# Kernel tuning notes

Hardware: AMD Instinct MI355X
Metric: run time of the kernel (lower is better)

Reference implementation:

```python
import jax, jax.numpy as jnp
import numpy as np

B, NQ, C, H0, NKPT, NH, NS = 8, 100, 768, 64, 17, 8, 3
HID = 4 * C
SIGMAS = (0.05, 0.15, 0.3)


def _ln(x, g, b):
    m = jnp.mean(x, -1, keepdims=True)
    v = jnp.mean((x - m) ** 2, -1, keepdims=True)
    return (x - m) / jnp.sqrt(v + 1e-5) * g + b


def _bias(kpts, H, W, sigma):
    # kpts: [B,N,2] normalized xy; returns additive bias [B,1,1,H*W]
    k = jnp.clip(kpts, 0.0, 1.0)
    ys, xs = jnp.meshgrid(jnp.arange(H, dtype=k.dtype), jnp.arange(W, dtype=k.dtype), indexing='ij')
    grid = jnp.stack([xs / (W - 1), ys / (H - 1)], -1).reshape(1, 1, H * W, 2)
    d = jnp.sum((k[:, :, None, :] - grid) ** 2, -1)  # [B,N,HW]
    m = jnp.min(d, axis=1)                           # [B,HW] min over keypoints
    return jnp.maximum(-(m / (2.0 * sigma * sigma)), -10000.0)[:, None, None, :]


def _attn(q, kv, Wq, bq, Wk, bk, Wv, bv, Wo, bo, bias, h):
    Bq, Nq, Cd = q.shape
    d = Cd // h
    scale = d ** -0.5
    qh = (q @ Wq + bq).reshape(Bq, Nq, h, d).transpose(0, 2, 1, 3)
    kh = (kv @ Wk + bk).reshape(Bq, -1, h, d).transpose(0, 2, 1, 3)
    vh = (kv @ Wv + bv).reshape(Bq, -1, h, d).transpose(0, 2, 1, 3)
    s = jnp.einsum('bhqd,bhkd->bhqk', qh, kh) * scale + bias
    a = jax.nn.softmax(s, axis=-1)
    o = jnp.einsum('bhqk,bhkd->bhqd', a, vh).transpose(0, 2, 1, 3).reshape(Bq, Nq, Cd)
    return o @ Wo + bo


def setup_inputs() -> dict:
    key = jax.random.key(0)
    def n(i, shape, sc=0.02):
        return jax.random.normal(jax.random.fold_in(key, i), shape, dtype=jnp.float32) * sc
    return dict(
        query_token=n(0, (B, NQ, C), 1.0),
        image_features=n(1, (B, C, H0, H0), 1.0),
        pose_kpts=jax.random.uniform(jax.random.fold_in(key, 2), (B, NKPT, 2), dtype=jnp.float32),
        norm_feat_g=jnp.ones((C,), jnp.float32), norm_feat_b=jnp.zeros((C,), jnp.float32),
        ds_w=n(3, (NS - 1, C, C, 2, 2)), ds_b=jnp.zeros((NS - 1, C), jnp.float32),
        q_w=n(4, (NS, C, C)), q_b=jnp.zeros((NS, C), jnp.float32),
        k_w=n(5, (NS, C, C)), k_b=jnp.zeros((NS, C), jnp.float32),
        v_w=n(6, (NS, C, C)), v_b=jnp.zeros((NS, C), jnp.float32),
        o_w=n(7, (NS, C, C)), o_b=jnp.zeros((NS, C), jnp.float32),
        scale_weights=jnp.ones((NS,), jnp.float32),
        norm_attn_g=jnp.ones((C,), jnp.float32), norm_attn_b=jnp.zeros((C,), jnp.float32),
        ffn_w1=n(8, (C, HID)), ffn_b1=jnp.zeros((HID,), jnp.float32),
        ffn_w2=n(9, (HID, C)), ffn_b2=jnp.zeros((C,), jnp.float32),
        norm_ffn_g=jnp.ones((C,), jnp.float32), norm_ffn_b=jnp.zeros((C,), jnp.float32),
    )


def reference(query_token, image_features, pose_kpts, norm_feat_g, norm_feat_b, ds_w, ds_b,
              q_w, q_b, k_w, k_b, v_w, v_b, o_w, o_b, scale_weights,
              norm_attn_g, norm_attn_b, ffn_w1, ffn_b1, ffn_w2, ffn_b2,
              norm_ffn_g, norm_ffn_b):
    w = jax.nn.softmax(scale_weights)
    curr = image_features
    fused = 0.0
    for i in range(NS):
        if i > 0:
            curr = jax.lax.conv_general_dilated(
                curr, ds_w[i - 1], (2, 2), 'VALID',
                dimension_numbers=('NCHW', 'OIHW', 'NCHW')) + ds_b[i - 1][None, :, None, None]
        Bc, Cc, Hc, Wc = curr.shape
        feat = _ln(curr.reshape(Bc, Cc, Hc * Wc).transpose(0, 2, 1), norm_feat_g, norm_feat_b)
        bias = _bias(pose_kpts, Hc, Wc, SIGMAS[min(i, len(SIGMAS) - 1)])
        fused = fused + w[i] * _attn(query_token, feat, q_w[i], q_b[i], k_w[i], k_b[i],
                                     v_w[i], v_b[i], o_w[i], o_b[i], bias, NH)
    x = _ln(query_token + fused, norm_attn_g, norm_attn_b)
    x = x + (jax.nn.relu(x @ ffn_w1 + ffn_b1) @ ffn_w2 + ffn_b2)
    return _ln(x, norm_ffn_g, norm_ffn_b)
```

## Files before the change

### kernel.cpp

```cpp
#include <hip/hip_runtime.h>
#include <stdint.h>


typedef unsigned short u16;
typedef __attribute__((ext_vector_type(4))) float f32x4;
typedef __attribute__((ext_vector_type(8))) short s16x8;
typedef __attribute__((ext_vector_type(4))) short s16x4;

#define DEVI static __device__ __forceinline__

DEVI float bf2f(u16 u){ union { unsigned int ui; float f; } v; v.ui = ((unsigned int)u)<<16; return v.f; }
DEVI u16 f2bf(float f){ union { float f; unsigned int ui; } v; v.f = f;
  unsigned int r = v.ui + 0x7FFFu + ((v.ui>>16)&1u); return (u16)(r>>16); }
DEVI f32x4 mfma_bf16(s16x8 a, s16x8 b, f32x4 c){
  return __builtin_amdgcn_mfma_f32_16x16x32_bf16(a,b,c,0,0,0);
}
DEVI void gload_lds16(const void* g, void* l){
  __builtin_amdgcn_global_load_lds((const __attribute__((address_space(1))) void*)g,
                                   (__attribute__((address_space(3))) void*)l, 16, 0, 0);
}


__global__ __launch_bounds__(64) void smax3_k(const float* __restrict__ sw, float* __restrict__ w3){
  if (threadIdx.x==0){
    float a=sw[0],b=sw[1],c=sw[2];
    float mx=fmaxf(a,fmaxf(b,c));
    float ea=__expf(a-mx), eb=__expf(b-mx), ec=__expf(c-mx);
    float inv=1.f/(ea+eb+ec);
    w3[0]=ea*inv; w3[1]=eb*inv; w3[2]=ec*inv;
  }
}

__global__ __launch_bounds__(256) void cvt_k(const float* __restrict__ in, u16* __restrict__ out, int n4){
  int i = blockIdx.x*256 + threadIdx.x;
  if (i>=n4) return;
  f32x4 v = *(const f32x4*)(in + (long)i*4);
  s16x4 o;
  o[0]=(short)f2bf(v[0]); o[1]=(short)f2bf(v[1]); o[2]=(short)f2bf(v[2]); o[3]=(short)f2bf(v[3]);
  *(s16x4*)(out + (long)i*4) = o;
}

__global__ __launch_bounds__(256) void tr_k(const float* __restrict__ in, u16* __restrict__ out, int R, int C){
  __shared__ float tile[32][33];
  long z = blockIdx.z;
  in  += z*(long)R*C;
  out += z*(long)R*C;
  int tx = threadIdx.x & 31, ty = threadIdx.x>>5;
  int r0 = blockIdx.y*32, c0 = blockIdx.x*32;
#pragma unroll
  for (int j=0;j<4;++j) tile[ty+j*8][tx] = in[(long)(r0+ty+j*8)*C + c0+tx];
  __syncthreads();
#pragma unroll
  for (int j=0;j<4;++j) out[(long)(c0+ty+j*8)*R + r0+tx] = f2bf(tile[tx][ty+j*8]);
}

__global__ __launch_bounds__(256) void convw_k(const float* __restrict__ dsw, u16* __restrict__ out){
  int i = blockIdx.x*256 + threadIdx.x;
  f32x4 v = *(const f32x4*)(dsw + (long)i*4);
  int s = i/(768*768); int rem = i - s*768*768;
  int o = rem/768; int ii = rem - o*768;
#pragma unroll
  for (int dyx=0;dyx<4;++dyx)
    out[(((long)s*4+dyx)*768 + o)*768 + ii] = f2bf(v[dyx]);
}

__global__ __launch_bounds__(256) void ln_bf16_k(const u16* __restrict__ in, u16* __restrict__ out,
    const float* __restrict__ g, const float* __restrict__ bt, int nrows){
  int w = threadIdx.x>>6, lane = threadIdx.x&63;
  long row = (long)blockIdx.x*4 + w;
  if (row >= nrows) return;
  const u16* rp = in + row*768;
  s16x8 v8 = *(const s16x8*)(rp + lane*8);
  s16x4 v4 = *(const s16x4*)(rp + 512 + lane*4);
  float x[12];
#pragma unroll
  for (int i=0;i<8;++i) x[i]   = bf2f((u16)v8[i]);
#pragma unroll
  for (int i=0;i<4;++i) x[8+i] = bf2f((u16)v4[i]);
  float s=0.f,s2=0.f;
#pragma unroll
  for (int i=0;i<12;++i){ s += x[i]; s2 += x[i]*x[i]; }
  for (int m=1;m<64;m<<=1){ s += __shfl_xor(s,m); s2 += __shfl_xor(s2,m); }
  float mean = s*(1.f/768.f);
  float var  = s2*(1.f/768.f) - mean*mean;
  float rstd = rsqrtf(fmaxf(var,0.f)+1e-5f);
  u16* op = out + row*768;
  s16x8 o8; s16x4 o4;
#pragma unroll
  for (int i=0;i<8;++i){ int c = lane*8+i;     o8[i] = (short)f2bf((x[i]-mean)*rstd*g[c]+bt[c]); }
#pragma unroll
  for (int i=0;i<4;++i){ int c = 512+lane*4+i; o4[i] = (short)f2bf((x[8+i]-mean)*rstd*g[c]+bt[c]); }
  *(s16x8*)(op + lane*8) = o8;
  *(s16x4*)(op + 512 + lane*4) = o4;
}

__global__ __launch_bounds__(256) void bias_k(const float* __restrict__ kpts, float* __restrict__ out,
    int HW, int log2W, float invWm1, float invHm1, float inv2s2){
  __shared__ float2 kp[17];
  int b = blockIdx.y;
  if (threadIdx.x < 17) kp[threadIdx.x] = ((const float2*)kpts)[b*17 + threadIdx.x];
  __syncthreads();
  int p = blockIdx.x*256 + threadIdx.x;
  int W = 1<<log2W;
  int y = p>>log2W, x = p&(W-1);
  float gx = x*invWm1, gy = y*invHm1;
  float m = 1e30f;
#pragma unroll 1
  for (int k=0;k<17;++k){
    float kx = fminf(fmaxf(kp[k].x,0.f),1.f) - gx;
    float ky = fminf(fmaxf(kp[k].y,0.f),1.f) - gy;
    m = fminf(m, kx*kx+ky*ky);
  }
  out[(long)b*HW + p] = fmaxf(-m*inv2s2, -10000.f);
}

template<int OUTM, bool RELU, bool QPAD, bool CONV>
__global__ __launch_bounds__(256,4) void gemm_k(
    const u16* __restrict__ A, const u16* __restrict__ Bt,
    const float* __restrict__ bias, void* __restrict__ Cout,
    int M, int N, int K,
    const float* __restrict__ alpha_ptr, int accum_init,
    int Win, int HWin, int log2Wout, int log2HWout, int ldct)
{
  __shared__ u16 As[2][128*32];
  __shared__ u16 Bs[2][128*32];
  const int t = threadIdx.x, lane = t&63, w = t>>6;
  const int wr = w>>1, wc = w&1;
  const int m0 = blockIdx.x*128, n0 = blockIdx.y*128;
  f32x4 acc[4][4];
  const f32x4 fz = {0.f,0.f,0.f,0.f};
#pragma unroll
  for (int i=0;i<4;++i)
#pragma unroll
    for (int j=0;j<4;++j) acc[i][j] = fz;

  const int nk = K>>5;
  const int nt = (CONV ? 4*nk : nk);

  auto stage = [&](int dyx, int k0, int b){
    const u16* Bp = CONV ? (Bt + (long)dyx*N*K) : Bt;
    const int dy = dyx>>1, dx = dyx&1;
#pragma unroll
    for (int p=0;p<2;++p){
      int f = p*256+t, r = f>>2, cv = f&3;
      int cvs = cv ^ ((r>>1)&3);
      int gm = m0 + r;
      long arow;
      if (CONV){
        int bb = gm >> log2HWout;
        int pp = gm & ((1<<log2HWout)-1);
        int yy = pp >> log2Wout, xx = pp & ((1<<log2Wout)-1);
        arow = (long)bb*HWin + (2*yy+dy)*Win + (2*xx+dx);
      } else arow = gm;
      gload_lds16(A + arow*(long)K + k0 + cvs*8, &As[b][(long)f*8]);
    }
#pragma unroll
    for (int p=0;p<2;++p){
      int f = p*256+t, r = f>>2, cv = f&3;
      int cvs = cv ^ ((r>>1)&3);
      gload_lds16(Bp + (long)(n0+r)*K + k0 + cvs*8, &Bs[b][(long)f*8]);
    }
  };

  stage(0, 0, 0);
  __syncthreads();

  int cur = 0, dyx = 0, kk = 0;
  for (int s = 0; s < nt; ++s){
    int nkk = kk + 1, ndx = dyx;
    if (nkk == nk){ nkk = 0; ndx = dyx + 1; }
    if (s + 1 < nt) stage(ndx, nkk<<5, cur^1);

    const int g16 = lane>>4, l16 = lane&15;
    s16x8 af[4], bf[4];
#pragma unroll
    for (int i=0;i<4;++i){
      int row = wr*64 + i*16 + l16;
      af[i] = *(const s16x8*)&As[cur][row*32 + ((g16 ^ ((row>>1)&3))*8)];
    }
#pragma unroll
    for (int j=0;j<4;++j){
      int row = wc*64 + j*16 + l16;
      bf[j] = *(const s16x8*)&Bs[cur][row*32 + ((g16 ^ ((row>>1)&3))*8)];
    }
#pragma unroll
    for (int i=0;i<4;++i)
#pragma unroll
      for (int j=0;j<4;++j)
        acc[i][j] = mfma_bf16(af[i], bf[j], acc[i][j]);

    __syncthreads();
    cur ^= 1; kk = nkk; dyx = ndx;
  }

  const int col16 = lane&15, g = lane>>4;
  float alpha = (OUTM==2) ? *alpha_ptr : 1.f;
#pragma unroll
  for (int i=0;i<4;++i){
    int rowbase = m0 + wr*64 + i*16 + g*4;
#pragma unroll
    for (int j=0;j<4;++j){
      int colg = n0 + wc*64 + j*16 + col16;
      float bv = bias ? bias[colg] : 0.f;
      f32x4 c = acc[i][j];
      if (OUTM==3){
        if (rowbase < M){
          int bb  = rowbase >> log2HWout;
          int pix = rowbase & ((1<<log2HWout)-1);
          s16x4 pk;
          pk[0]=(short)f2bf(c[0]+bv); pk[1]=(short)f2bf(c[1]+bv);
          pk[2]=(short)f2bf(c[2]+bv); pk[3]=(short)f2bf(c[3]+bv);
          *(s16x4*)((u16*)Cout + ((long)bb*768 + colg)*ldct + pix) = pk;
        }
      } else {
#pragma unroll
        for (int r=0;r<4;++r){
          int row = rowbase + r;
          if (row < M){
            float v = c[r] + bv;
            if (RELU) v = fmaxf(v, 0.f);
            if (OUTM==0){
              long orow = row;
              if (QPAD){ int bb = row/100; orow = bb*128 + (row - bb*100); }
              ((u16*)Cout)[orow*(long)N + colg] = f2bf(v);
            } else if (OUTM==1){
              ((float*)Cout)[(long)row*N + colg] = v;
            } else {
              float* p = (float*)Cout + (long)row*N + colg;
              *p = (accum_init ? 0.f : *p) + alpha*v;
            }
          }
        }
      }
    }
  }
}

__global__ __launch_bounds__(256,2) void attn_fwd_k(
    const u16* __restrict__ Qp, const u16* __restrict__ Kb,
    const u16* __restrict__ Vt, const float* __restrict__ biasb,
    float* __restrict__ Opart, float* __restrict__ mpart, float* __restrict__ lpart,
    int HW, int ntiles)
{
  __shared__ u16 Ps[4*32*64];
  const int t = threadIdx.x, lane = t&63, w = t>>6;
  const int col = lane&15, g = lane>>4;
  const int bh = blockIdx.x, b = bh>>3, h = bh&7, ch = blockIdx.y;
  const int kvbase = ch*ntiles*64;
  const int qrow = w*32;
  const u16* Qbase = Qp + (long)b*128*768 + h*96;
  const u16* Kbase = Kb + (long)b*HW*768 + h*96;
  const u16* Vbase = Vt + ((long)b*768 + h*96)*HW;
  const float* bb  = biasb + (long)b*HW;
  const float scale = 0.10206207261596575f;

  s16x8 qf[2][3];
#pragma unroll
  for (int qi=0;qi<2;++qi)
#pragma unroll
    for (int kf=0;kf<3;++kf)
      qf[qi][kf] = *(const s16x8*)(Qbase + (long)(qrow+qi*16+col)*768 + kf*32 + g*8);

  const f32x4 fz = {0.f,0.f,0.f,0.f};
  f32x4 of[2][6];
#pragma unroll
  for (int qi=0;qi<2;++qi)
#pragma unroll
    for (int nf=0;nf<6;++nf) of[qi][nf] = fz;
  float mrow[2][4], lrow[2][4];
#pragma unroll
  for (int qi=0;qi<2;++qi)
#pragma unroll
    for (int r=0;r<4;++r){ mrow[qi][r] = -1e30f; lrow[qi][r] = 0.f; }

  for (int ti=0; ti<ntiles; ++ti){
    const int kv0 = kvbase + ti*64;
    s16x8 kfr[4][3];
#pragma unroll
    for (int cf=0;cf<4;++cf)
#pragma unroll
      for (int kf=0;kf<3;++kf)
        kfr[cf][kf] = *(const s16x8*)(Kbase + (long)(kv0+cf*16+col)*768 + kf*32 + g*8);
    f32x4 sc[2][4];
#pragma unroll
    for (int qi=0;qi<2;++qi)
#pragma unroll
      for (int cf=0;cf<4;++cf) sc[qi][cf] = fz;
#pragma unroll
    for (int kf=0;kf<3;++kf)
#pragma unroll
      for (int qi=0;qi<2;++qi)
#pragma unroll
        for (int cf=0;cf<4;++cf)
          sc[qi][cf] = mfma_bf16(qf[qi][kf], kfr[cf][kf], sc[qi][cf]);
    float bv[4];
#pragma unroll
    for (int cf=0;cf<4;++cf) bv[cf] = bb[kv0+cf*16+col];

#pragma unroll
    for (int qi=0;qi<2;++qi){
      f32x4 sp[4];
#pragma unroll
      for (int cf=0;cf<4;++cf)
#pragma unroll
        for (int r=0;r<4;++r) sp[cf][r] = sc[qi][cf][r]*scale + bv[cf];
      f32x4 mx = sp[0];
#pragma unroll
      for (int cf=1;cf<4;++cf)
#pragma unroll
        for (int r=0;r<4;++r) mx[r] = fmaxf(mx[r], sp[cf][r]);
      for (int mm=1;mm<16;mm<<=1){
#pragma unroll
        for (int r=0;r<4;++r) mx[r] = fmaxf(mx[r], __shfl_xor(mx[r], mm));
      }
      float sf[4], mn[4];
#pragma unroll
      for (int r=0;r<4;++r){
        mn[r] = fmaxf(mrow[qi][r], mx[r]);
        sf[r] = __expf(mrow[qi][r]-mn[r]);
        mrow[qi][r] = mn[r];
      }
      f32x4 psum = fz;
#pragma unroll
      for (int cf=0;cf<4;++cf)
#pragma unroll
        for (int r=0;r<4;++r){ float p = __expf(sp[cf][r]-mn[r]); sp[cf][r]=p; psum[r]+=p; }
      for (int mm=1;mm<16;mm<<=1){
#pragma unroll
        for (int r=0;r<4;++r) psum[r] += __shfl_xor(psum[r], mm);
      }
#pragma unroll
      for (int r=0;r<4;++r) lrow[qi][r] = lrow[qi][r]*sf[r] + psum[r];
#pragma unroll
      for (int nf=0;nf<6;++nf)
#pragma unroll
        for (int r=0;r<4;++r) of[qi][nf][r] *= sf[r];
#pragma unroll
      for (int cf=0;cf<4;++cf)
#pragma unroll
        for (int r=0;r<4;++r){
          int lr = qi*16 + g*4 + r;
          int cc = cf*16 + col;
          int byteoff = (qrow + lr)*128 + ((cc*2) ^ ((lr&7)<<4));
          *(u16*)((char*)Ps + byteoff) = f2bf(sp[cf][r]);
        }
    }
#pragma unroll
    for (int k2=0;k2<2;++k2){
      s16x8 pa[2];
#pragma unroll
      for (int qi=0;qi<2;++qi){
        int lr = qi*16 + col;
        int byteoff = (qrow+lr)*128 + ((k2*64 + g*16) ^ ((lr&7)<<4));
        pa[qi] = *(const s16x8*)((const char*)Ps + byteoff);
      }
#pragma unroll
      for (int nf=0;nf<6;++nf){
        s16x8 vbf = *(const s16x8*)(Vbase + (long)(nf*16+col)*HW + kv0 + k2*32 + g*8);
#pragma unroll
        for (int qi=0;qi<2;++qi)
          of[qi][nf] = mfma_bf16(pa[qi], vbf, of[qi][nf]);
      }
    }
  }
  long obase = ((long)ch*64 + bh)*128;
#pragma unroll
  for (int qi=0;qi<2;++qi)
#pragma unroll
    for (int nf=0;nf<6;++nf)
#pragma unroll
      for (int r=0;r<4;++r)
        Opart[(obase + qrow + qi*16 + g*4 + r)*96L + nf*16 + col] = of[qi][nf][r];
  if (col==0){
#pragma unroll
    for (int qi=0;qi<2;++qi)
#pragma unroll
      for (int r=0;r<4;++r){
        int row = qrow + qi*16 + g*4 + r;
        mpart[obase+row] = mrow[qi][r];
        lpart[obase+row] = lrow[qi][r];
      }
  }
}

__global__ __launch_bounds__(128) void attn_comb_k(const float* __restrict__ Opart,
    const float* __restrict__ mpart, const float* __restrict__ lpart,
    u16* __restrict__ out, int nch){
  int bh = blockIdx.x, q = blockIdx.y, d = threadIdx.x;
  int b = bh>>3, h = bh&7;
  float M = -1e30f;
  for (int c=0;c<nch;++c) M = fmaxf(M, mpart[((long)c*64+bh)*128+q]);
  float L = 0.f, o = 0.f;
  for (int c=0;c<nch;++c){
    long base = ((long)c*64+bh)*128+q;
    float e = __expf(mpart[base]-M);
    L += lpart[base]*e;
    if (d<96) o += Opart[base*96+d]*e;
  }
  if (d<96) out[((long)(b*100+q))*768 + h*96 + d] = f2bf(o/L);
}

__global__ __launch_bounds__(256) void postattn_k(const float* __restrict__ q,
    const float* __restrict__ fus, const float* __restrict__ g, const float* __restrict__ bt,
    float* __restrict__ x1f, u16* __restrict__ x1b){
  int w = threadIdx.x>>6, lane = threadIdx.x&63;
  long row = (long)blockIdx.x*4 + w;
  const f32x4* qp = (const f32x4*)(q   + row*768);
  const f32x4* fp = (const f32x4*)(fus + row*768);
  f32x4 xv[3];
  float s=0.f,s2=0.f;
#pragma unroll
  for (int p=0;p<3;++p){
    f32x4 a = qp[p*64+lane], c = fp[p*64+lane];
    xv[p] = a + c;
#pragma unroll
    for (int r=0;r<4;++r){ s += xv[p][r]; s2 += xv[p][r]*xv[p][r]; }
  }
  for (int m=1;m<64;m<<=1){ s += __shfl_xor(s,m); s2 += __shfl_xor(s2,m); }
  float mean = s*(1.f/768.f);
  float var  = s2*(1.f/768.f) - mean*mean;
  float rstd = rsqrtf(fmaxf(var,0.f)+1e-5f);
#pragma unroll
  for (int p=0;p<3;++p){
    int c0 = (p*64+lane)*4;
    f32x4 o; s16x4 ob;
#pragma unroll
    for (int r=0;r<4;++r){ o[r] = (xv[p][r]-mean)*rstd*g[c0+r]+bt[c0+r]; ob[r]=(short)f2bf(o[r]); }
    *(f32x4*)(x1f + row*768 + c0) = o;
    *(s16x4*)(x1b + row*768 + c0) = ob;
  }
}

__global__ __launch_bounds__(256) void final_k(const float* __restrict__ x1f,
    const float* __restrict__ yb, const float* __restrict__ g, const float* __restrict__ bt,
    float* __restrict__ out){
  int w = threadIdx.x>>6, lane = threadIdx.x&63;
  long row = (long)blockIdx.x*4 + w;
  const f32x4* xp = (const f32x4*)(x1f + row*768);
  const f32x4* yp = (const f32x4*)(yb  + row*768);
  f32x4 xv[3];
  float s=0.f,s2=0.f;
#pragma unroll
  for (int p=0;p<3;++p){
    f32x4 a = xp[p*64+lane], c = yp[p*64+lane];
    xv[p] = a + c;
#pragma unroll
    for (int r=0;r<4;++r){ s += xv[p][r]; s2 += xv[p][r]*xv[p][r]; }
  }
  for (int m=1;m<64;m<<=1){ s += __shfl_xor(s,m); s2 += __shfl_xor(s2,m); }
  float mean = s*(1.f/768.f);
  float var  = s2*(1.f/768.f) - mean*mean;
  float rstd = rsqrtf(fmaxf(var,0.f)+1e-5f);
#pragma unroll
  for (int p=0;p<3;++p){
    int c0 = (p*64+lane)*4;
    f32x4 o;
#pragma unroll
    for (int r=0;r<4;++r) o[r] = (xv[p][r]-mean)*rstd*g[c0+r]+bt[c0+r];
    *(f32x4*)(out + row*768 + c0) = o;
  }
}

extern "C" void kernel_launch(void* const* d_in, const int* in_sizes, int n_in,
                              void* d_out, int out_size, void* d_ws, size_t ws_size,
                              hipStream_t stream)
{
  (void)in_sizes; (void)n_in; (void)out_size; (void)ws_size;
  const float* query = (const float*)d_in[0];
  const float* imgf  = (const float*)d_in[1];
  const float* kpts  = (const float*)d_in[2];
  const float* nfg   = (const float*)d_in[3];
  const float* nfb   = (const float*)d_in[4];
  const float* dsw   = (const float*)d_in[5];
  const float* dsb   = (const float*)d_in[6];
  const float* qw    = (const float*)d_in[7];
  const float* qbv   = (const float*)d_in[8];
  const float* kw    = (const float*)d_in[9];
  const float* kbv   = (const float*)d_in[10];
  const float* vw    = (const float*)d_in[11];
  const float* vbv   = (const float*)d_in[12];
  const float* ow    = (const float*)d_in[13];
  const float* obv   = (const float*)d_in[14];
  const float* sw    = (const float*)d_in[15];
  const float* nag   = (const float*)d_in[16];
  const float* nab   = (const float*)d_in[17];
  const float* fw1   = (const float*)d_in[18];
  const float* fb1   = (const float*)d_in[19];
  const float* fw2   = (const float*)d_in[20];
  const float* fb2   = (const float*)d_in[21];
  const float* ngg   = (const float*)d_in[22];
  const float* ngb   = (const float*)d_in[23];
  float* out = (float*)d_out;

  char* ws = (char*)d_ws;
  size_t off = 0;
  auto carve = [&](size_t bytes)->char*{
    off = (off + 255) & ~(size_t)255;
    char* p = ws + off; off += bytes; return p;
  };
  float* w3     = (float*)carve(16);
  u16* wq_t     = (u16*)carve(3UL*768*768*2);
  u16* wk_t     = (u16*)carve(3UL*768*768*2);
  u16* wv_t     = (u16*)carve(3UL*768*768*2);
  u16* wo_t     = (u16*)carve(3UL*768*768*2);
  u16* wf1_t    = (u16*)carve(3072UL*768*2);
  u16* wf2_t    = (u16*)carve(768UL*3072*2);
  u16* wcv_t    = (u16*)carve(2UL*4*768*768*2);
  u16* qbf      = (u16*)carve(896UL*768*2);
  u16* Qpad     = (u16*)carve(8UL*128*768*2);
  u16* curr0    = (u16*)carve(8UL*4096*768*2);
  u16* curr1    = (u16*)carve(8UL*1024*768*2);
  u16* curr2    = (u16*)carve(8UL*256*768*2);
  u16* feat     = (u16*)carve(8UL*4096*768*2);
  u16* Kb       = (u16*)carve(8UL*4096*768*2);
  u16* Vt       = (u16*)carve(8UL*768*4096*2);
  float* biasb  = (float*)carve(8UL*4096*4);
  float* Opart  = (float*)carve(8UL*64*128*96*4);
  float* mpart  = (float*)carve(8UL*64*128*4);
  float* lpart  = (float*)carve(8UL*64*128*4);
  u16* attnO    = (u16*)carve(896UL*768*2);
  float* fusedb = (float*)carve(800UL*768*4);
  float* x1f    = (float*)carve(800UL*768*4);
  u16* x1b      = (u16*)carve(896UL*768*2);
  u16* hb       = (u16*)carve(896UL*3072*2);
  float* yb     = (float*)carve(800UL*768*4);

  hipMemsetAsync(Qpad, 0, 8UL*128*768*2, stream);
  smax3_k<<<1,64,0,stream>>>(sw, w3);
  cvt_k<<<600,256,0,stream>>>(query, qbf, 153600);
  tr_k<<<dim3(24,24,3),256,0,stream>>>(qw, wq_t, 768, 768);
  tr_k<<<dim3(24,24,3),256,0,stream>>>(kw, wk_t, 768, 768);
  tr_k<<<dim3(24,24,3),256,0,stream>>>(vw, wv_t, 768, 768);
  tr_k<<<dim3(24,24,3),256,0,stream>>>(ow, wo_t, 768, 768);
  tr_k<<<dim3(96,24,1),256,0,stream>>>(fw1, wf1_t, 768, 3072);
  tr_k<<<dim3(24,96,1),256,0,stream>>>(fw2, wf2_t, 3072, 768);
  convw_k<<<4608,256,0,stream>>>(dsw, wcv_t);
  tr_k<<<dim3(128,24,8),256,0,stream>>>(imgf, curr0, 768, 4096);

  const int HWs[3]    = {4096,1024,256};
  const int log2Ws[3] = {6,5,4};
  const int chunks[3] = {8,4,2};
  const float sig[3]  = {0.05f,0.15f,0.3f};
  u16* currp[3] = {curr0, curr1, curr2};

  for (int s=0;s<3;++s){
    int HW = HWs[s], W = 1<<log2Ws[s];
    int M = 8*HW;
    if (s>0){
      int HWin = HWs[s-1], Win = 1<<log2Ws[s-1];
      gemm_k<0,false,false,true><<<dim3(M/128,6),256,0,stream>>>(
        currp[s-1], wcv_t + (long)(s-1)*4*768*768, dsb + (s-1)*768, currp[s],
        M, 768, 768, nullptr, 0,
        Win, HWin, log2Ws[s], 2*log2Ws[s], 0);
    }
    ln_bf16_k<<<M/4,256,0,stream>>>(currp[s], feat, nfg, nfb, M);
    gemm_k<0,false,false,false><<<dim3(M/128,6),256,0,stream>>>(
      feat, wk_t + (long)s*768*768, kbv + s*768, Kb, M, 768, 768,
      nullptr, 0, 0,0,0,0,0);
    gemm_k<3,false,false,false><<<dim3(M/128,6),256,0,stream>>>(
      feat, wv_t + (long)s*768*768, vbv + s*768, Vt, M, 768, 768,
      nullptr, 0, 0,0,0, 2*log2Ws[s], HW);
    gemm_k<0,false,true,false><<<dim3(7,6),256,0,stream>>>(
      qbf, wq_t + (long)s*768*768, qbv + s*768, Qpad, 800, 768, 768,
      nullptr, 0, 0,0,0,0,0);
    float inv2s2 = 1.f/(2.f*sig[s]*sig[s]);
    float invWm1 = 1.f/(float)(W-1);
    bias_k<<<dim3(HW/256,8),256,0,stream>>>(kpts, biasb, HW, log2Ws[s], invWm1, invWm1, inv2s2);
    attn_fwd_k<<<dim3(64,chunks[s]),256,0,stream>>>(
      Qpad, Kb, Vt, biasb, Opart, mpart, lpart, HW, (HW/64)/chunks[s]);
    attn_comb_k<<<dim3(64,100),128,0,stream>>>(Opart, mpart, lpart, attnO, chunks[s]);
    gemm_k<2,false,false,false><<<dim3(7,6),256,0,stream>>>(
      attnO, wo_t + (long)s*768*768, obv + s*768, fusedb, 800, 768, 768,
      w3+s, (s==0)?1:0, 0,0,0,0,0);
  }

  postattn_k<<<200,256,0,stream>>>(query, fusedb, nag, nab, x1f, x1b);
  gemm_k<0,true,false,false><<<dim3(7,24),256,0,stream>>>(
    x1b, wf1_t, fb1, hb, 800, 3072, 768, nullptr, 0, 0,0,0,0,0);
  gemm_k<1,false,false,false><<<dim3(7,6),256,0,stream>>>(
    hb, wf2_t, fb2, yb, 800, 768, 3072, nullptr, 0, 0,0,0,0,0);
  final_k<<<200,256,0,stream>>>(x1f, yb, ngg, ngb, out);
}
```

Before: 1.091 ms.

## Precompute GEMM load offsets and use partial vmcnt waits for double buffering

```diff
diff --git a/kernel.cpp b/kernel.cpp
--- a/kernel.cpp
+++ b/kernel.cpp
@@ -136,40 +136,54 @@
 
   const int nk = K>>5;
   const int nt = (CONV ? 4*nk : nk);
+  const long NK = (long)N*K;
+
+  long aoff[2], boff[2];
+  long abase0 = 0, abase1 = 0;
+#pragma unroll
+  for (int p=0;p<2;++p){
+    int f = p*256+t, r = f>>2, cv = f&3;
+    int cvs = cv ^ ((r>>1)&3);
+    int gm = m0 + r;
+    if (CONV){
+      int bb = gm >> log2HWout;
+      int pp = gm & ((1<<log2HWout)-1);
+      int yy = pp >> log2Wout, xx = pp & ((1<<log2Wout)-1);
+      long ab = (long)bb*HWin + 2*yy*(long)Win + 2*xx;
+      if (p==0) abase0 = ab; else abase1 = ab;
+      aoff[p] = (long)cvs*8;
+    } else {
+      aoff[p] = (long)gm*K + cvs*8;
+    }
+    boff[p] = (long)(n0+r)*K + cvs*8;
+  }
 
   auto stage = [&](int dyx, int k0, int b){
-    const u16* Bp = CONV ? (Bt + (long)dyx*N*K) : Bt;
-    const int dy = dyx>>1, dx = dyx&1;
+    long bdy = CONV ? (long)dyx*NK : 0;
+    long adel = 0;
+    if (CONV) adel = ((long)(dyx>>1)*Win + (dyx&1))*(long)K;
 #pragma unroll
     for (int p=0;p<2;++p){
-      int f = p*256+t, r = f>>2, cv = f&3;
-      int cvs = cv ^ ((r>>1)&3);
-      int gm = m0 + r;
-      long arow;
-      if (CONV){
-        int bb = gm >> log2HWout;
-        int pp = gm & ((1<<log2HWout)-1);
-        int yy = pp >> log2Wout, xx = pp & ((1<<log2Wout)-1);
-        arow = (long)bb*HWin + (2*yy+dy)*Win + (2*xx+dx);
-      } else arow = gm;
-      gload_lds16(A + arow*(long)K + k0 + cvs*8, &As[b][(long)f*8]);
-    }
-#pragma unroll
-    for (int p=0;p<2;++p){
-      int f = p*256+t, r = f>>2, cv = f&3;
-      int cvs = cv ^ ((r>>1)&3);
-      gload_lds16(Bp + (long)(n0+r)*K + k0 + cvs*8, &Bs[b][(long)f*8]);
+      long ao = CONV ? (((p==0)?abase0:abase1)*(long)K + adel + aoff[p]) : aoff[p];
+      gload_lds16(A + ao + k0, &As[b][(long)(p*256+t)*8]);
+      gload_lds16(Bt + boff[p] + bdy + k0, &Bs[b][(long)(p*256+t)*8]);
     }
   };
 
   stage(0, 0, 0);
-  __syncthreads();
 
   int cur = 0, dyx = 0, kk = 0;
   for (int s = 0; s < nt; ++s){
     int nkk = kk + 1, ndx = dyx;
     if (nkk == nk){ nkk = 0; ndx = dyx + 1; }
-    if (s + 1 < nt) stage(ndx, nkk<<5, cur^1);
+    if (s + 1 < nt){
+      stage(ndx, nkk<<5, cur^1);
+      asm volatile("s_waitcnt vmcnt(4)" ::: "memory");
+    } else {
+      asm volatile("s_waitcnt vmcnt(0)" ::: "memory");
+    }
+    __builtin_amdgcn_s_barrier();
+    __builtin_amdgcn_sched_barrier(0);
 
     const int g16 = lane>>4, l16 = lane&15;
     s16x8 af[4], bf[4];
@@ -189,7 +203,8 @@
       for (int j=0;j<4;++j)
         acc[i][j] = mfma_bf16(af[i], bf[j], acc[i][j]);
 
-    __syncthreads();
+    __builtin_amdgcn_sched_barrier(0);
+    __builtin_amdgcn_s_barrier();
     cur ^= 1; kk = nkk; dyx = ndx;
   }
 
```

New measurement: 1.138 ms. +4.4%, slower.
